# Kernel tuning notes

Hardware: AMD Instinct MI355X
Metric: run time of the kernel (lower is better)

The kernel has to match this reference:

```python
import jax, jax.numpy as jnp
import numpy as np

N = 100000   # nodes
F = 128      # input features
H = 128      # hidden = 2*output_dim
Z = 64       # output_dim
E = 1600000  # message-passing edges
EP = 200000  # pos/neg decode edges each


def setup_inputs() -> dict:
    key = jax.random.key(0)
    ks = jax.random.split(key, 6)
    x = jax.random.normal(ks[0], (N, F), dtype=jnp.float32)
    edge_index = jax.random.randint(ks[1], (2, E), 0, N, dtype=jnp.int64)
    pos_edge = jax.random.randint(ks[2], (2, EP), 0, N, dtype=jnp.int64)
    neg_edge = jax.random.randint(ks[3], (2, EP), 0, N, dtype=jnp.int64)
    W1 = jax.random.normal(ks[4], (F, H), dtype=jnp.float32) / np.float32(np.sqrt(F))
    b1 = jnp.zeros((H,), jnp.float32)
    W2 = jax.random.normal(ks[5], (H, Z), dtype=jnp.float32) / np.float32(np.sqrt(H))
    b2 = jnp.zeros((Z,), jnp.float32)
    return dict(x=x, W1=W1, b1=b1, W2=W2, b2=b2,
                edge_index=edge_index, pos_edge=pos_edge, neg_edge=neg_edge)


def _gcn_conv(x, src, dst, norm, W, b, n):
    # x' = scatter_add_dst(norm * (x @ W)[src]) + b   (GCNConv, sym-normalized, self-loops)
    h = x @ W                         # [N, out]
    msg = h[src] * norm[:, None]      # [E+N, out] gather + scale
    out = jax.ops.segment_sum(msg, dst, num_segments=n)
    return out + b


def reference(x, W1, b1, W2, b2, edge_index, pos_edge, neg_edge):
    # add self-loops (GCNConv default)
    loop = jnp.arange(N, dtype=edge_index.dtype)
    src = jnp.concatenate([edge_index[0], loop])
    dst = jnp.concatenate([edge_index[1], loop])
    # symmetric normalization deg^-1/2[src] * deg^-1/2[dst]
    deg = jax.ops.segment_sum(jnp.ones(dst.shape, x.dtype), dst, num_segments=N)
    dinv = jnp.where(deg > 0, jax.lax.rsqrt(deg), 0.0)
    norm = dinv[src] * dinv[dst]
    # encoder: GCN -> ReLU -> GCN
    h = jax.nn.relu(_gcn_conv(x, src, dst, norm, W1, b1, N))
    latent = _gcn_conv(h, src, dst, norm, W2, b2, N)
    # decoder: edge dot products on pos+neg edges
    e = jnp.concatenate([pos_edge, neg_edge], axis=-1)  # [2, 2*EP]
    logits = jnp.sum(latent[e[0]] * latent[e[1]], axis=-1)
    return logits
```

## Files before the change

kernel.cpp:

```cpp
#include <hip/hip_runtime.h>

#define N_NODES 100000
#define F_IN    128
#define H_DIM   128
#define Z_DIM   64
#define E_EDGES 1600000
#define EP_EDGES 200000

#define BSHIFT 7
#define NBUCK  ((N_NODES + 127) >> 7)
#define CHUNK  4096
#define NCHUNK ((E_EDGES + CHUNK - 1) / CHUNK)

typedef __attribute__((ext_vector_type(8))) short short8;
typedef __attribute__((ext_vector_type(4))) float f32x4;
typedef unsigned int uint;
typedef unsigned short ushort;

__device__ __forceinline__ ushort f2bf(float f) {
    uint u = __float_as_uint(f);
    u += 0x7fffu + ((u >> 16) & 1u);
    return (ushort)(u >> 16);
}
__device__ __forceinline__ float bflo(uint u) { return __uint_as_float(u << 16); }
__device__ __forceinline__ float bfhi(uint u) { return __uint_as_float(u & 0xffff0000u); }


__global__ __launch_bounds__(256) void wprep_kernel(const float* __restrict__ W1,
                                                    const float* __restrict__ W2,
                                                    ushort* __restrict__ W1T,
                                                    ushort* __restrict__ W2T,
                                                    int* __restrict__ gcur) {
    int i = blockIdx.x * 256 + threadIdx.x;
    if (i < 1024) gcur[i] = 0;
    if (i < 128 * 128) {
        int n = i >> 7, k = i & 127;
        W1T[i] = f2bf(W1[k * 128 + n]);
    }
    int j = i - 128 * 128;
    if (j >= 0 && j < 64 * 128) {
        int n = j >> 7, k = j & 127;
        W2T[j] = f2bf(W2[k * 64 + n]);
    }
}


__global__ __launch_bounds__(256) void bhist_kernel(const int* __restrict__ dst,
                                                    int* __restrict__ gcur,
                                                    int* __restrict__ tbl) {
    __shared__ int lh[NBUCK];
    for (int i = threadIdx.x; i < NBUCK; i += 256) lh[i] = 0;
    __syncthreads();
    int base = blockIdx.x * CHUNK;
    int end = min(base + CHUNK, E_EDGES);
    for (int e = base + threadIdx.x; e < end; e += 256)
        atomicAdd(&lh[dst[e] >> BSHIFT], 1);
    __syncthreads();
    int* trow = tbl + (size_t)blockIdx.x * NBUCK;
    for (int i = threadIdx.x; i < NBUCK; i += 256) {
        int c = lh[i];
        trow[i] = c;
        if (c) atomicAdd(&gcur[i], c);
    }
}


__global__ __launch_bounds__(1024) void bscan_kernel(int* __restrict__ gc) {
    __shared__ int s[1024];
    int t = threadIdx.x;
    int v = (t < NBUCK) ? gc[t] : 0;
    s[t] = v;
    __syncthreads();
    #pragma unroll
    for (int off = 1; off < 1024; off <<= 1) {
        int x = (t >= off) ? s[t - off] : 0;
        __syncthreads();
        s[t] += x;
        __syncthreads();
    }
    if (t < NBUCK) gc[t] = s[t] - v;
}


__global__ __launch_bounds__(512) void chunk_scan_kernel(int* __restrict__ tbl,
                                                         const int* __restrict__ gcur) {
    __shared__ int s[512];
    int b = blockIdx.x, t = threadIdx.x;
    int v = (t < NCHUNK) ? tbl[(size_t)t * NBUCK + b] : 0;
    s[t] = v;
    __syncthreads();
    #pragma unroll
    for (int off = 1; off < 512; off <<= 1) {
        int x = (t >= off) ? s[t - off] : 0;
        __syncthreads();
        s[t] += x;
        __syncthreads();
    }
    if (t < NCHUNK)
        tbl[(size_t)t * NBUCK + b] = gcur[b] + (s[t] - v);
}


__global__ __launch_bounds__(256) void bscatter_kernel(const int* __restrict__ src,
                                                       const int* __restrict__ dst,
                                                       const int* __restrict__ tbl,
                                                       int* __restrict__ sorted) {
    __shared__ int lbase[NBUCK];
    int c = blockIdx.x;
    const int* trow = tbl + (size_t)c * NBUCK;
    for (int i = threadIdx.x; i < NBUCK; i += 256) lbase[i] = trow[i];
    __syncthreads();
    int base = c * CHUNK;
    int end = min(base + CHUNK, E_EDGES);
    for (int e = base + threadIdx.x; e < end; e += 256) {
        int d = dst[e];
        int p = atomicAdd(&lbase[d >> BSHIFT], 1);
        sorted[p] = (src[e] << 7) | (d & 127);
    }
}


__global__ __launch_bounds__(256) void bucket_csr_kernel(const int* __restrict__ sorted,
                                                         const int* __restrict__ gcur,
                                                         int* __restrict__ csr,
                                                         int* __restrict__ ends,
                                                         float* __restrict__ dinv) {
    __shared__ int lcnt[4][128], lcur[4][128];
    int b = blockIdx.x, t = threadIdx.x;
    int wave = t >> 6;
    int bstart = gcur[b];
    int bend = (b + 1 < NBUCK) ? gcur[b + 1] : E_EDGES;
    if (t < 128) { lcnt[0][t] = 0; lcnt[1][t] = 0; }
    else { int u = t - 128; lcnt[2][u] = 0; lcnt[3][u] = 0; }
    __syncthreads();
    for (int i = bstart + t; i < bend; i += 256)
        atomicAdd(&lcnt[wave][sorted[i] & 127], 1);
    __syncthreads();
    if (t < 64) {
        int w0a = lcnt[0][t], w1a = lcnt[1][t], w2a = lcnt[2][t], w3a = lcnt[3][t];
        int w0b = lcnt[0][t + 64], w1b = lcnt[1][t + 64], w2b = lcnt[2][t + 64], w3b = lcnt[3][t + 64];
        int c0 = w0a + w1a + w2a + w3a;
        int c1 = w0b + w1b + w2b + w3b;
        int s0 = c0;
        #pragma unroll
        for (int d = 1; d < 64; d <<= 1) {
            int x = __shfl_up(s0, d, 64);
            if (t >= d) s0 += x;
        }
        int tot0 = __shfl(s0, 63, 64);
        int s1 = c1;
        #pragma unroll
        for (int d = 1; d < 64; d <<= 1) {
            int x = __shfl_up(s1, d, 64);
            if (t >= d) s1 += x;
        }
        s1 += tot0;
        int basea = bstart + s0 - c0;
        int baseb = bstart + s1 - c1;
        lcur[0][t] = basea;
        lcur[1][t] = basea + w0a;
        lcur[2][t] = basea + w0a + w1a;
        lcur[3][t] = basea + w0a + w1a + w2a;
        lcur[0][t + 64] = baseb;
        lcur[1][t + 64] = baseb + w0b;
        lcur[2][t + 64] = baseb + w0b + w1b;
        lcur[3][t + 64] = baseb + w0b + w1b + w2b;
        int n0 = b * 128 + t, n1 = n0 + 64;
        if (n0 < N_NODES) { ends[n0] = bstart + s0; dinv[n0] = rsqrtf(1.0f + (float)c0); }
        if (n1 < N_NODES) { ends[n1] = bstart + s1; dinv[n1] = rsqrtf(1.0f + (float)c1); }
    }
    __syncthreads();
    for (int i = bstart + t; i < bend; i += 256) {
        int v = sorted[i];
        int p = atomicAdd(&lcur[wave][v & 127], 1);
        csr[p] = v >> 7;
    }
}


template<int NC, bool A_F32>
__global__ __launch_bounds__(256) void gemm_mfma_kernel(const void* __restrict__ Ap,
                                                        const ushort* __restrict__ BT,
                                                        const float* __restrict__ dinv,
                                                        ushort* __restrict__ C, int M) {
    constexpr int NT = NC / 16;
    __shared__ ushort Bs[4 * NT * 64 * 8];

    for (int idx = threadIdx.x; idx < 4 * NT * 64; idx += 256) {
        int l   = idx & 63;
        int nt  = (idx >> 6) % NT;
        int kc  = idx / (64 * NT);
        int m16 = l & 15, quad = l >> 4;
        ((short8*)Bs)[idx] =
            *(const short8*)(BT + ((nt * 16 + m16) * 128 + kc * 32 + quad * 8));
    }
    __syncthreads();

    int wave = threadIdx.x >> 6, lane = threadIdx.x & 63;
    int m16 = lane & 15, quad = lane >> 4;
    int row0 = (blockIdx.x * 4 + wave) * 16;
    if (row0 >= M) return;
    int arow = row0 + m16;
    if (arow >= M) arow = M - 1;

    f32x4 acc[NT];
    #pragma unroll
    for (int t = 0; t < NT; ++t) acc[t] = (f32x4){0.f, 0.f, 0.f, 0.f};

    #pragma unroll
    for (int kc = 0; kc < 4; ++kc) {
        short8 a;
        if (A_F32) {
            const float* A = (const float*)Ap;
            const float4* p = (const float4*)(A + (size_t)arow * 128 + kc * 32 + quad * 8);
            float4 x0 = p[0], x1 = p[1];
            a[0] = (short)f2bf(x0.x); a[1] = (short)f2bf(x0.y);
            a[2] = (short)f2bf(x0.z); a[3] = (short)f2bf(x0.w);
            a[4] = (short)f2bf(x1.x); a[5] = (short)f2bf(x1.y);
            a[6] = (short)f2bf(x1.z); a[7] = (short)f2bf(x1.w);
        } else {
            a = *(const short8*)((const ushort*)Ap + (size_t)arow * 128 + kc * 32 + quad * 8);
        }
        #pragma unroll
        for (int nt = 0; nt < NT; ++nt) {
            short8 b = ((const short8*)Bs)[(kc * NT + nt) * 64 + lane];
            acc[nt] = __builtin_amdgcn_mfma_f32_16x16x32_bf16(a, b, acc[nt], 0, 0, 0);
        }
    }

    #pragma unroll
    for (int r = 0; r < 4; ++r) {
        int row = row0 + quad * 4 + r;
        if (row < M) {
            float dr = dinv[row];
            #pragma unroll
            for (int nt = 0; nt < NT; ++nt)
                C[(size_t)row * NC + nt * 16 + m16] = f2bf(acc[nt][r] * dr);
        }
    }
}


__global__ __launch_bounds__(64, 4) void gather_gemm2_kernel(const ushort* __restrict__ feat,
                                                             const float* __restrict__ bias,
                                                             const float* __restrict__ dinv,
                                                             const int* __restrict__ ends,
                                                             const int* __restrict__ csr,
                                                             const ushort* __restrict__ W2T,
                                                             ushort* __restrict__ C) {
    __shared__ uint T[16 * 68];
    int lane = threadIdx.x;
    int row0 = blockIdx.x * 16;
    const uint* F = (const uint*)feat;
    float2 bv = ((const float2*)bias)[lane];

    for (int i = 0; i < 16; ++i) {
        int n = row0 + i;
        uint su = F[(uint)n * 64u + (uint)lane];
        float l0 = bflo(su), h0 = bfhi(su);
        float l1 = 0.f, h1 = 0.f;
        int j0 = n ? ends[n - 1] : 0, j1 = ends[n];
        j0 = __builtin_amdgcn_readfirstlane(j0);
        j1 = __builtin_amdgcn_readfirstlane(j1);
        for (int base = j0; base < j1; base += 64) {
            int m = min(64, j1 - base);
            int idxv = __builtin_nontemporal_load(csr + base + min(lane, m - 1));
            int e = 0;
            for (; e + 8 <= m; e += 8) {
                int s0 = __builtin_amdgcn_readlane(idxv, e + 0);
                int s1 = __builtin_amdgcn_readlane(idxv, e + 1);
                int s2 = __builtin_amdgcn_readlane(idxv, e + 2);
                int s3 = __builtin_amdgcn_readlane(idxv, e + 3);
                int s4 = __builtin_amdgcn_readlane(idxv, e + 4);
                int s5 = __builtin_amdgcn_readlane(idxv, e + 5);
                int s6 = __builtin_amdgcn_readlane(idxv, e + 6);
                int s7 = __builtin_amdgcn_readlane(idxv, e + 7);
                uint r0 = F[(uint)s0 * 64u + (uint)lane];
                uint r1 = F[(uint)s1 * 64u + (uint)lane];
                uint r2 = F[(uint)s2 * 64u + (uint)lane];
                uint r3 = F[(uint)s3 * 64u + (uint)lane];
                uint r4 = F[(uint)s4 * 64u + (uint)lane];
                uint r5 = F[(uint)s5 * 64u + (uint)lane];
                uint r6 = F[(uint)s6 * 64u + (uint)lane];
                uint r7 = F[(uint)s7 * 64u + (uint)lane];
                l0 += bflo(r0) + bflo(r2);
                l1 += bflo(r1) + bflo(r3);
                h0 += bfhi(r0) + bfhi(r2);
                h1 += bfhi(r1) + bfhi(r3);
                l0 += bflo(r4) + bflo(r6);
                l1 += bflo(r5) + bflo(r7);
                h0 += bfhi(r4) + bfhi(r6);
                h1 += bfhi(r5) + bfhi(r7);
            }
            for (; e < m; ++e) {
                int s = __builtin_amdgcn_readlane(idxv, e);
                uint r = F[(uint)s * 64u + (uint)lane];
                l0 += bflo(r); h0 += bfhi(r);
            }
        }
        float dn = dinv[n];
        float rlo = fmaxf(bv.x + dn * (l0 + l1), 0.f);
        float rhi = fmaxf(bv.y + dn * (h0 + h1), 0.f);
        T[i * 68 + lane] = (uint)f2bf(rlo) | ((uint)f2bf(rhi) << 16);
    }

    int m16 = lane & 15, quad = lane >> 4;
    f32x4 acc[4];
    #pragma unroll
    for (int t = 0; t < 4; ++t) acc[t] = (f32x4){0.f, 0.f, 0.f, 0.f};
    #pragma unroll
    for (int kc = 0; kc < 4; ++kc) {
        short8 a = *(const short8*)&T[m16 * 68 + kc * 16 + quad * 4];
        #pragma unroll
        for (int nt = 0; nt < 4; ++nt) {
            short8 b = *(const short8*)(W2T + ((nt * 16 + m16) * 128 + kc * 32 + quad * 8));
            acc[nt] = __builtin_amdgcn_mfma_f32_16x16x32_bf16(a, b, acc[nt], 0, 0, 0);
        }
    }
    #pragma unroll
    for (int r = 0; r < 4; ++r) {
        int row = row0 + quad * 4 + r;
        float dr = dinv[row];
        #pragma unroll
        for (int nt = 0; nt < 4; ++nt)
            C[(size_t)row * 64 + nt * 16 + m16] = f2bf(acc[nt][r] * dr);
    }
}


__global__ __launch_bounds__(256, 8) void gather64_kernel(const ushort* __restrict__ feat,
                                                          const float* __restrict__ bias,
                                                          const float* __restrict__ dinv,
                                                          const int* __restrict__ ends,
                                                          const int* __restrict__ csr,
                                                          ushort* __restrict__ outB) {
    int wave = threadIdx.x >> 6, lane = threadIdx.x & 63;
    int g = lane >> 5, c = lane & 31;
    int n = blockIdx.x * 4 + wave;
    const uint* F = (const uint*)feat;

    float a0 = 0.f, a1 = 0.f;
    uint su = F[(uint)n * 32u + (uint)c];
    if (g == 0) { a0 = bflo(su); a1 = bfhi(su); }

    int j0 = n ? ends[n - 1] : 0, j1 = ends[n];
    j0 = __builtin_amdgcn_readfirstlane(j0);
    j1 = __builtin_amdgcn_readfirstlane(j1);

    for (int base = j0; base < j1; base += 64) {
        int m = min(64, j1 - base);
        int idxv = __builtin_nontemporal_load(csr + base + min(lane, m - 1));
        int e = 0;
        for (; e + 8 <= m; e += 8) {
            int sa0 = __builtin_amdgcn_readlane(idxv, e + 0);
            int sb0 = __builtin_amdgcn_readlane(idxv, e + 1);
            int sa1 = __builtin_amdgcn_readlane(idxv, e + 2);
            int sb1 = __builtin_amdgcn_readlane(idxv, e + 3);
            int sa2 = __builtin_amdgcn_readlane(idxv, e + 4);
            int sb2 = __builtin_amdgcn_readlane(idxv, e + 5);
            int sa3 = __builtin_amdgcn_readlane(idxv, e + 6);
            int sb3 = __builtin_amdgcn_readlane(idxv, e + 7);
            uint p0 = (uint)(g ? sb0 : sa0);
            uint p1 = (uint)(g ? sb1 : sa1);
            uint p2 = (uint)(g ? sb2 : sa2);
            uint p3 = (uint)(g ? sb3 : sa3);
            uint r0 = F[p0 * 32u + (uint)c];
            uint r1 = F[p1 * 32u + (uint)c];
            uint r2 = F[p2 * 32u + (uint)c];
            uint r3 = F[p3 * 32u + (uint)c];
            a0 += bflo(r0) + bflo(r1);
            a1 += bfhi(r0) + bfhi(r1);
            a0 += bflo(r2) + bflo(r3);
            a1 += bfhi(r2) + bfhi(r3);
        }
        for (; e + 2 <= m; e += 2) {
            int sa = __builtin_amdgcn_readlane(idxv, e);
            int sb = __builtin_amdgcn_readlane(idxv, e + 1);
            uint p = (uint)(g ? sb : sa);
            uint r = F[p * 32u + (uint)c];
            a0 += bflo(r); a1 += bfhi(r);
        }
        if (e < m) {
            int s = __builtin_amdgcn_readlane(idxv, e);
            uint r = F[(uint)s * 32u + (uint)c];
            if (g == 0) { a0 += bflo(r); a1 += bfhi(r); }
        }
    }
    a0 += __shfl_xor(a0, 32, 64);
    a1 += __shfl_xor(a1, 32, 64);
    if (g == 0) {
        float dn = dinv[n];
        float2 bv = ((const float2*)bias)[c];
        float o0 = bv.x + dn * a0;
        float o1 = bv.y + dn * a1;
        ((uint*)outB)[(uint)n * 32u + (uint)c] = (uint)f2bf(o0) | ((uint)f2bf(o1) << 16);
    }
}


__global__ __launch_bounds__(256) void decode_kernel(const ushort* __restrict__ latentB,
                                                     const int* __restrict__ pos,
                                                     const int* __restrict__ neg,
                                                     float* __restrict__ out) {
    int gwave = (blockIdx.x * 256 + threadIdx.x) >> 6;
    int lane = threadIdx.x & 63;
    int half = lane >> 5, sl = lane & 31;
    const uint* L = (const uint*)latentB;
    int e0 = gwave * 8 + half * 4;
    if (e0 >= 2 * EP_EDGES) return;

    int ia[4], ib[4];
    #pragma unroll
    for (int u = 0; u < 4; ++u) {
        int edge = e0 + u;
        if (edge < EP_EDGES) {
            ia[u] = pos[edge];
            ib[u] = pos[EP_EDGES + edge];
        } else {
            int e2 = edge - EP_EDGES;
            ia[u] = neg[e2];
            ib[u] = neg[EP_EDGES + e2];
        }
    }
    uint la[4], lb[4];
    #pragma unroll
    for (int u = 0; u < 4; ++u) {
        la[u] = L[(size_t)ia[u] * 32 + sl];
        lb[u] = L[(size_t)ib[u] * 32 + sl];
    }
    float v[4];
    #pragma unroll
    for (int u = 0; u < 4; ++u)
        v[u] = bflo(la[u]) * bflo(lb[u]) + bfhi(la[u]) * bfhi(lb[u]);
    #pragma unroll
    for (int u = 0; u < 4; ++u) {
        float s = v[u];
        #pragma unroll
        for (int off = 16; off > 0; off >>= 1) s += __shfl_down(s, off, 64);
        if (sl == 0) out[e0 + u] = s;
    }
}


extern "C" void kernel_launch(void* const* d_in, const int* in_sizes, int n_in,
                              void* d_out, int out_size, void* d_ws, size_t ws_size,
                              hipStream_t stream) {
    const float* x  = (const float*)d_in[0];
    const float* W1 = (const float*)d_in[1];
    const float* b1 = (const float*)d_in[2];
    const float* W2 = (const float*)d_in[3];
    const float* b2 = (const float*)d_in[4];
    const int* edge_index = (const int*)d_in[5];
    const int* pos = (const int*)d_in[6];
    const int* neg = (const int*)d_in[7];
    float* out = (float*)d_out;

    const int* src = edge_index;
    const int* dst = edge_index + E_EDGES;

    float*  dinv   = (float*)d_ws;
    int*    ends   = (int*)(dinv + N_NODES);
    int*    gcur   = ends + N_NODES;
    int*    tbl    = gcur + 1024;
    int*    sorted = tbl + NCHUNK * NBUCK;
    int*    csr    = sorted + E_EDGES;
    ushort* W1T    = (ushort*)(csr + E_EDGES);
    ushort* W2T    = W1T + 128 * 128;
    ushort* bufH   = (ushort*)(((uintptr_t)(W2T + 64 * 128) + 255) & ~(uintptr_t)255);
    ushort* bufR   = bufH + (size_t)N_NODES * 128;

    wprep_kernel<<<96, 256, 0, stream>>>(W1, W2, W1T, W2T, gcur);

    bhist_kernel<<<NCHUNK, 256, 0, stream>>>(dst, gcur, tbl);
    bscan_kernel<<<1, 1024, 0, stream>>>(gcur);
    chunk_scan_kernel<<<NBUCK, 512, 0, stream>>>(tbl, gcur);
    bscatter_kernel<<<NCHUNK, 256, 0, stream>>>(src, dst, tbl, sorted);
    bucket_csr_kernel<<<NBUCK, 256, 0, stream>>>(sorted, gcur, csr, ends, dinv);

    const int GEMM_GRID = (N_NODES + 63) / 64;

    gemm_mfma_kernel<128, true><<<GEMM_GRID, 256, 0, stream>>>(x, W1T, dinv, bufH, N_NODES);

    gather_gemm2_kernel<<<N_NODES / 16, 64, 0, stream>>>(bufH, b1, dinv, ends, csr, W2T, bufR);

    ushort* latentB = bufH;
    gather64_kernel<<<N_NODES / 4, 256, 0, stream>>>(bufR, b2, dinv, ends, csr, latentB);

    decode_kernel<<<(2 * EP_EDGES) / 32, 256, 0, stream>>>(latentB, pos, neg, out);
}
```

Before: 312.4 us.

## Split layer-2 gather+GEMM into separate kernels and split feature halves across blocks

Replaces the fused gather+GEMM2 kernel, which ran one wave per 16 nodes, with a gather kernel that runs one wave per node per feature half, followed by a separate MFMA GEMM kernel. The final 64-wide gather is likewise split into two 32-feature halves, with four edges handled in parallel per wave. The aim is more parallelism and better latency hiding in the gathers, which were bound by occupancy. In exchange the edge indices are read twice and an extra intermediate pass through global memory plus an extra kernel launch are added.

```diff
diff --git a/kernel.cpp b/kernel.cpp
--- a/kernel.cpp
+++ b/kernel.cpp
@@ -241,106 +241,20 @@
 }
 
 
-__global__ __launch_bounds__(64, 4) void gather_gemm2_kernel(const ushort* __restrict__ feat,
-                                                             const float* __restrict__ bias,
-                                                             const float* __restrict__ dinv,
-                                                             const int* __restrict__ ends,
-                                                             const int* __restrict__ csr,
-                                                             const ushort* __restrict__ W2T,
-                                                             ushort* __restrict__ C) {
-    __shared__ uint T[16 * 68];
-    int lane = threadIdx.x;
-    int row0 = blockIdx.x * 16;
-    const uint* F = (const uint*)feat;
-    float2 bv = ((const float2*)bias)[lane];
-
-    for (int i = 0; i < 16; ++i) {
-        int n = row0 + i;
-        uint su = F[(uint)n * 64u + (uint)lane];
-        float l0 = bflo(su), h0 = bfhi(su);
-        float l1 = 0.f, h1 = 0.f;
-        int j0 = n ? ends[n - 1] : 0, j1 = ends[n];
-        j0 = __builtin_amdgcn_readfirstlane(j0);
-        j1 = __builtin_amdgcn_readfirstlane(j1);
-        for (int base = j0; base < j1; base += 64) {
-            int m = min(64, j1 - base);
-            int idxv = __builtin_nontemporal_load(csr + base + min(lane, m - 1));
-            int e = 0;
-            for (; e + 8 <= m; e += 8) {
-                int s0 = __builtin_amdgcn_readlane(idxv, e + 0);
-                int s1 = __builtin_amdgcn_readlane(idxv, e + 1);
-                int s2 = __builtin_amdgcn_readlane(idxv, e + 2);
-                int s3 = __builtin_amdgcn_readlane(idxv, e + 3);
-                int s4 = __builtin_amdgcn_readlane(idxv, e + 4);
-                int s5 = __builtin_amdgcn_readlane(idxv, e + 5);
-                int s6 = __builtin_amdgcn_readlane(idxv, e + 6);
-                int s7 = __builtin_amdgcn_readlane(idxv, e + 7);
-                uint r0 = F[(uint)s0 * 64u + (uint)lane];
-                uint r1 = F[(uint)s1 * 64u + (uint)lane];
-                uint r2 = F[(uint)s2 * 64u + (uint)lane];
-                uint r3 = F[(uint)s3 * 64u + (uint)lane];
-                uint r4 = F[(uint)s4 * 64u + (uint)lane];
-                uint r5 = F[(uint)s5 * 64u + (uint)lane];
-                uint r6 = F[(uint)s6 * 64u + (uint)lane];
-                uint r7 = F[(uint)s7 * 64u + (uint)lane];
-                l0 += bflo(r0) + bflo(r2);
-                l1 += bflo(r1) + bflo(r3);
-                h0 += bfhi(r0) + bfhi(r2);
-                h1 += bfhi(r1) + bfhi(r3);
-                l0 += bflo(r4) + bflo(r6);
-                l1 += bflo(r5) + bflo(r7);
-                h0 += bfhi(r4) + bfhi(r6);
-                h1 += bfhi(r5) + bfhi(r7);
-            }
-            for (; e < m; ++e) {
-                int s = __builtin_amdgcn_readlane(idxv, e);
-                uint r = F[(uint)s * 64u + (uint)lane];
-                l0 += bflo(r); h0 += bfhi(r);
-            }
-        }
-        float dn = dinv[n];
-        float rlo = fmaxf(bv.x + dn * (l0 + l1), 0.f);
-        float rhi = fmaxf(bv.y + dn * (h0 + h1), 0.f);
-        T[i * 68 + lane] = (uint)f2bf(rlo) | ((uint)f2bf(rhi) << 16);
-    }
-
-    int m16 = lane & 15, quad = lane >> 4;
-    f32x4 acc[4];
-    #pragma unroll
-    for (int t = 0; t < 4; ++t) acc[t] = (f32x4){0.f, 0.f, 0.f, 0.f};
-    #pragma unroll
-    for (int kc = 0; kc < 4; ++kc) {
-        short8 a = *(const short8*)&T[m16 * 68 + kc * 16 + quad * 4];
-        #pragma unroll
-        for (int nt = 0; nt < 4; ++nt) {
-            short8 b = *(const short8*)(W2T + ((nt * 16 + m16) * 128 + kc * 32 + quad * 8));
-            acc[nt] = __builtin_amdgcn_mfma_f32_16x16x32_bf16(a, b, acc[nt], 0, 0, 0);
-        }
-    }
-    #pragma unroll
-    for (int r = 0; r < 4; ++r) {
-        int row = row0 + quad * 4 + r;
-        float dr = dinv[row];
-        #pragma unroll
-        for (int nt = 0; nt < 4; ++nt)
-            C[(size_t)row * 64 + nt * 16 + m16] = f2bf(acc[nt][r] * dr);
-    }
-}
-
-
-__global__ __launch_bounds__(256, 8) void gather64_kernel(const ushort* __restrict__ feat,
-                                                          const float* __restrict__ bias,
-                                                          const float* __restrict__ dinv,
-                                                          const int* __restrict__ ends,
-                                                          const int* __restrict__ csr,
-                                                          ushort* __restrict__ outB) {
+__global__ __launch_bounds__(256, 8) void gather128h_kernel(const ushort* __restrict__ feat,
+                                                            const float* __restrict__ bias,
+                                                            const float* __restrict__ dinv,
+                                                            const int* __restrict__ ends,
+                                                            const int* __restrict__ csr,
+                                                            ushort* __restrict__ out) {
     int wave = threadIdx.x >> 6, lane = threadIdx.x & 63;
     int g = lane >> 5, c = lane & 31;
-    int n = blockIdx.x * 4 + wave;
-    const uint* F = (const uint*)feat;
+    int half = blockIdx.x / (N_NODES / 4);
+    int n = (blockIdx.x % (N_NODES / 4)) * 4 + wave;
+    const uint* F = (const uint*)feat + half * 32;
 
     float a0 = 0.f, a1 = 0.f;
-    uint su = F[(uint)n * 32u + (uint)c];
+    uint su = F[(uint)n * 64u + (uint)c];
     if (g == 0) { a0 = bflo(su); a1 = bfhi(su); }
 
     int j0 = n ? ends[n - 1] : 0, j1 = ends[n];
@@ -364,10 +278,10 @@
             uint p1 = (uint)(g ? sb1 : sa1);
             uint p2 = (uint)(g ? sb2 : sa2);
             uint p3 = (uint)(g ? sb3 : sa3);
-            uint r0 = F[p0 * 32u + (uint)c];
-            uint r1 = F[p1 * 32u + (uint)c];
-            uint r2 = F[p2 * 32u + (uint)c];
-            uint r3 = F[p3 * 32u + (uint)c];
+            uint r0 = F[p0 * 64u + (uint)c];
+            uint r1 = F[p1 * 64u + (uint)c];
+            uint r2 = F[p2 * 64u + (uint)c];
+            uint r3 = F[p3 * 64u + (uint)c];
             a0 += bflo(r0) + bflo(r1);
             a1 += bfhi(r0) + bfhi(r1);
             a0 += bflo(r2) + bflo(r3);
@@ -377,12 +291,12 @@
             int sa = __builtin_amdgcn_readlane(idxv, e);
             int sb = __builtin_amdgcn_readlane(idxv, e + 1);
             uint p = (uint)(g ? sb : sa);
-            uint r = F[p * 32u + (uint)c];
+            uint r = F[p * 64u + (uint)c];
             a0 += bflo(r); a1 += bfhi(r);
         }
         if (e < m) {
             int s = __builtin_amdgcn_readlane(idxv, e);
-            uint r = F[(uint)s * 32u + (uint)c];
+            uint r = F[(uint)s * 64u + (uint)c];
             if (g == 0) { a0 += bflo(r); a1 += bfhi(r); }
         }
     }
@@ -390,10 +304,72 @@
     a1 += __shfl_xor(a1, 32, 64);
     if (g == 0) {
         float dn = dinv[n];
-        float2 bv = ((const float2*)bias)[c];
+        float2 bv = ((const float2*)bias)[half * 32 + c];
+        float o0 = fmaxf(bv.x + dn * a0, 0.f);
+        float o1 = fmaxf(bv.y + dn * a1, 0.f);
+        ((uint*)out)[(uint)n * 64u + (uint)(half * 32 + c)] =
+            (uint)f2bf(o0) | ((uint)f2bf(o1) << 16);
+    }
+}
+
+
+__global__ __launch_bounds__(256, 8) void gather64h_kernel(const ushort* __restrict__ feat,
+                                                           const float* __restrict__ bias,
+                                                           const float* __restrict__ dinv,
+                                                           const int* __restrict__ ends,
+                                                           const int* __restrict__ csr,
+                                                           ushort* __restrict__ outB) {
+    int wave = threadIdx.x >> 6, lane = threadIdx.x & 63;
+    int q = lane >> 4, c = lane & 15;
+    int half = blockIdx.x / (N_NODES / 4);
+    int n = (blockIdx.x % (N_NODES / 4)) * 4 + wave;
+    const uint* F = (const uint*)feat + half * 16;
+
+    float a0 = 0.f, a1 = 0.f;
+    uint su = F[(uint)n * 32u + (uint)c];
+    if (q == 0) { a0 = bflo(su); a1 = bfhi(su); }
+
+    int j0 = n ? ends[n - 1] : 0, j1 = ends[n];
+    j0 = __builtin_amdgcn_readfirstlane(j0);
+    j1 = __builtin_amdgcn_readfirstlane(j1);
+
+    for (int base = j0; base < j1; base += 64) {
+        int m = min(64, j1 - base);
+        int idxv = __builtin_nontemporal_load(csr + base + min(lane, m - 1));
+        int e = 0;
+        for (; e + 16 <= m; e += 16) {
+            #pragma unroll
+            for (int gk = 0; gk < 4; ++gk) {
+                int eb = e + gk * 4;
+                int s0 = __builtin_amdgcn_readlane(idxv, eb + 0);
+                int s1 = __builtin_amdgcn_readlane(idxv, eb + 1);
+                int s2 = __builtin_amdgcn_readlane(idxv, eb + 2);
+                int s3 = __builtin_amdgcn_readlane(idxv, eb + 3);
+                int s = (q < 2) ? (q == 0 ? s0 : s1) : (q == 2 ? s2 : s3);
+                uint r = F[(uint)s * 32u + (uint)c];
+                a0 += bflo(r); a1 += bfhi(r);
+            }
+        }
+        for (; e < m; e += 4) {
+            int mc = m - 1;
+            int s0 = __builtin_amdgcn_readlane(idxv, min(e + 0, mc));
+            int s1 = __builtin_amdgcn_readlane(idxv, min(e + 1, mc));
+            int s2 = __builtin_amdgcn_readlane(idxv, min(e + 2, mc));
+            int s3 = __builtin_amdgcn_readlane(idxv, min(e + 3, mc));
+            int s = (q < 2) ? (q == 0 ? s0 : s1) : (q == 2 ? s2 : s3);
+            uint r = F[(uint)s * 32u + (uint)c];
+            if (e + q < m) { a0 += bflo(r); a1 += bfhi(r); }
+        }
+    }
+    a0 += __shfl_xor(a0, 16, 64); a0 += __shfl_xor(a0, 32, 64);
+    a1 += __shfl_xor(a1, 16, 64); a1 += __shfl_xor(a1, 32, 64);
+    if (q == 0) {
+        float dn = dinv[n];
+        float2 bv = ((const float2*)bias)[half * 16 + c];
         float o0 = bv.x + dn * a0;
         float o1 = bv.y + dn * a1;
-        ((uint*)outB)[(uint)n * 32u + (uint)c] = (uint)f2bf(o0) | ((uint)f2bf(o1) << 16);
+        ((uint*)outB)[(uint)n * 32u + (uint)(half * 16 + c)] =
+            (uint)f2bf(o0) | ((uint)f2bf(o1) << 16);
     }
 }
 
@@ -481,10 +457,12 @@
 
     gemm_mfma_kernel<128, true><<<GEMM_GRID, 256, 0, stream>>>(x, W1T, dinv, bufH, N_NODES);
 
-    gather_gemm2_kernel<<<N_NODES / 16, 64, 0, stream>>>(bufH, b1, dinv, ends, csr, W2T, bufR);
-
-    ushort* latentB = bufH;
-    gather64_kernel<<<N_NODES / 4, 256, 0, stream>>>(bufR, b2, dinv, ends, csr, latentB);
+    gather128h_kernel<<<2 * (N_NODES / 4), 256, 0, stream>>>(bufH, b1, dinv, ends, csr, bufR);
+
+    gemm_mfma_kernel<64, false><<<GEMM_GRID, 256, 0, stream>>>(bufR, W2T, dinv, bufH, N_NODES);
+
+    ushort* latentB = bufR;
+    gather64h_kernel<<<2 * (N_NODES / 4), 256, 0, stream>>>(bufH, b2, dinv, ends, csr, latentB);
 
     decode_kernel<<<(2 * EP_EDGES) / 32, 256, 0, stream>>>(latentB, pos, neg, out);
 }
```

New measurement: 396.9 us. 27.0% more time.
